# Optimization experiments

Hardware: AMD Instinct MI355X
Metric: run time of the kernel (lower is better)

The kernel has to match this reference:

```python
import jax, jax.numpy as jnp
import numpy as np

K = 100  # number of negative samples
EPS = 1e-6


def setup_inputs() -> dict:
    key = jax.random.key(0)
    k1, k2, k3 = jax.random.split(key, 3)
    B, V = 1024, 100000
    noise_logits = jax.random.normal(k1, (B, V), dtype=jnp.float32)
    actual_logits = jax.random.normal(k2, (B, K + 1), dtype=jnp.float32)
    target_id = jax.random.randint(k3, (B,), 0, V, dtype=jnp.int64)
    return {"noise_logits": noise_logits, "actual_logits": actual_logits, "target_id": target_id}


def reference(noise_logits, actual_logits, target_id):
    B, V = noise_logits.shape
    # Mask the target item out (torch: one_hot scatter then softmax*one_hot, renormalized
    # implicitly by multinomial). Equivalent: set target logit to -inf.
    neg_inf = jnp.finfo(noise_logits.dtype).min
    masked = noise_logits.at[jnp.arange(B), target_id].set(neg_inf)
    # Without-replacement multinomial from softmax(masked) via Gumbel top-k.
    g = jax.random.gumbel(jax.random.key(42), (B, V), dtype=noise_logits.dtype)
    _, neg_items = jax.lax.top_k(masked + g, K)  # [B, K]
    pos_neg_items = jnp.concatenate([target_id[:, None].astype(neg_items.dtype), neg_items], axis=1)  # [B, K+1]
    # Scoring
    noise_prob = jnp.take_along_axis(noise_logits, pos_neg_items, axis=1)  # [B, K+1]
    noise_prob = jax.nn.softmax(noise_prob, axis=-1)
    actual_prob = jax.nn.softmax(actual_logits, axis=-1)
    deno = K * noise_prob + actual_prob + EPS
    tmp1 = actual_prob / deno
    tmp2 = noise_prob / deno
    likeli = jnp.concatenate([tmp1[:, :1], tmp2[:, 1:]], axis=1)
    likeli = jnp.where(likeli == 1.0, 1.0 + EPS, likeli)
    return -jnp.mean(jnp.log(likeli))
```

## Files before the change

kernel.cpp:

```cpp
#include <hip/hip_runtime.h>
#include <stdint.h>

#define NROWS   1024
#define NV      100000
#define NSEL    101
#define NBINS   2048
#define POOLSZ  2048
#define CHUNK   1024
#define NCHUNK  ((NV + CHUNK - 1) / CHUNK)

__device__ __forceinline__ uint32_t rotl32(uint32_t x, uint32_t r) {
  return (x << r) | (x >> (32u - r));
}

__device__ __forceinline__ uint32_t jax_random_bits(uint32_t n) {
  const uint32_t K1 = 42u;
  const uint32_t K2 = 0x1BD11BF0u;
  uint32_t x0 = 0u;
  uint32_t x1 = n + K1;
#define TF_R(r) { x0 += x1; x1 = rotl32(x1, (r)); x1 ^= x0; }
  TF_R(13u) TF_R(15u) TF_R(26u) TF_R(6u)
  x0 += K1; x1 += K2 + 1u;
  TF_R(17u) TF_R(29u) TF_R(16u) TF_R(24u)
  x0 += K2; x1 += 0u + 2u;
  TF_R(13u) TF_R(15u) TF_R(26u) TF_R(6u)
  x0 += 0u; x1 += K1 + 3u;
  TF_R(17u) TF_R(29u) TF_R(16u) TF_R(24u)
  x0 += K1; x1 += K2 + 4u;
  TF_R(13u) TF_R(15u) TF_R(26u) TF_R(6u)
  x0 += K2; x1 += 0u + 5u;
#undef TF_R
  return x0 ^ x1;
}

__device__ __forceinline__ float jax_gumbel(uint32_t n) {
  uint32_t bits = jax_random_bits(n);
  float f = __uint_as_float((bits >> 9) | 0x3f800000u) - 1.0f;
  f = fmaxf(f, 1.1754943508222875e-38f);
  return -__logf(-__logf(f));
}

__device__ __forceinline__ float blk_reduce(float x, int tid, float* wred, bool is_max) {
  #pragma unroll
  for (int off = 32; off >= 1; off >>= 1) {
    float o = __shfl_down(x, off);
    x = is_max ? fmaxf(x, o) : (x + o);
  }
  if ((tid & 63) == 0) wred[tid >> 6] = x;
  __syncthreads();
  float r;
  if (is_max) r = fmaxf(fmaxf(wred[0], wred[1]), fmaxf(wred[2], wred[3]));
  else        r = wred[0] + wred[1] + wred[2] + wred[3];
  __syncthreads();
  return r;
}

__device__ __forceinline__ uint32_t sortable_bin(float v) {
  uint32_t fb = __float_as_uint(v);
  uint32_t key = fb ^ (uint32_t)(((int32_t)fb >> 31) | (int32_t)0x80000000);
  return key >> 21;
}

__global__ void __launch_bounds__(256)
nce_row_kernel(const float* __restrict__ noise, const float* __restrict__ actual,
               const int* __restrict__ target, float* __restrict__ acc) {
  const int row = blockIdx.x;
  const int tid = threadIdx.x;

  __shared__ float    pv[POOLSZ];
  __shared__ uint32_t pi[POOLSZ];
  __shared__ uint32_t hist[NBINS];
  __shared__ uint32_t s_cnt;
  __shared__ uint32_t s_thr;
  __shared__ float    s_wred[4];

  for (int i = tid; i < NBINS; i += 256) hist[i] = 0u;
  if (tid == 0) { s_cnt = 0u; s_thr = 0u; }
  __syncthreads();

  const float* rowp = noise + (size_t)row * NV;
  const uint32_t tgt = (uint32_t)target[row];
  const uint32_t nbase = (uint32_t)row * (uint32_t)NV;

  for (int c = 0; c < NCHUNK; ++c) {
    const uint32_t thr = s_thr;
    const int v = c * CHUNK + tid * 4;
    if (v < NV) {
      float4 a = *reinterpret_cast<const float4*>(rowp + v);
      float av[4] = {a.x, a.y, a.z, a.w};
      #pragma unroll
      for (int j = 0; j < 4; ++j) {
        const uint32_t col = (uint32_t)(v + j);
        const float logit = (col == tgt) ? -3.4028234663852886e+38f : av[j];
        const float val = logit + jax_gumbel(nbase + col);
        const uint32_t bin = sortable_bin(val);
        if (bin >= thr) {
          uint32_t pos = atomicAdd(&s_cnt, 1u);
          if (pos < POOLSZ) { pv[pos] = val; pi[pos] = col; }
          atomicAdd(&hist[bin], 1u);
        }
      }
    }
    __syncthreads();

    if (tid < 64) {
      const int bpl = NBINS / 64;
      uint32_t sum = 0;
      const uint32_t base = (uint32_t)tid * bpl;
      #pragma unroll
      for (int j = 0; j < bpl; ++j) sum += hist[base + j];
      uint32_t suf = sum;
      #pragma unroll
      for (int off = 1; off < 64; off <<= 1) {
        uint32_t o = __shfl_down(suf, off);
        if (tid + off < 64) suf += o;
      }
      const uint32_t sufnext = suf - sum;
      if (suf >= 100u && sufnext < 100u) {
        uint32_t cum = sufnext;
        uint32_t b = base + bpl - 1;
        for (;; --b) { cum += hist[b]; if (cum >= 100u) break; }
        if (b > s_thr) s_thr = b;
      }
    }
    __syncthreads();

    if (s_cnt > (uint32_t)(POOLSZ - CHUNK)) {
      const uint32_t n = min(s_cnt, (uint32_t)POOLSZ);
      const uint32_t thr2 = s_thr;
      float    lv[8]; uint32_t li[8]; int nkeep = 0;
      for (uint32_t p = tid; p < n; p += 256) {
        float val = pv[p];
        if (sortable_bin(val) >= thr2) { lv[nkeep] = val; li[nkeep] = pi[p]; ++nkeep; }
      }
      __syncthreads();
      if (tid == 0) s_cnt = 0u;
      __syncthreads();
      for (int k = 0; k < nkeep; ++k) {
        uint32_t pos = atomicAdd(&s_cnt, 1u);
        if (pos < POOLSZ) { pv[pos] = lv[k]; pi[pos] = li[k]; }
      }
      __syncthreads();
    }
  }
  __syncthreads();

  const uint32_t n = min(s_cnt, (uint32_t)POOLSZ);
  uint32_t sortn = 128;
  while (sortn < n) sortn <<= 1;
  for (uint32_t i = n + tid; i < sortn; i += 256) { pv[i] = -INFINITY; pi[i] = 0xFFFFFFFFu; }
  __syncthreads();

  for (uint32_t ksz = 2; ksz <= sortn; ksz <<= 1) {
    for (uint32_t jsz = ksz >> 1; jsz >= 1; jsz >>= 1) {
      for (uint32_t i = tid; i < sortn; i += 256) {
        const uint32_t ixj = i ^ jsz;
        if (ixj > i) {
          const bool desc = ((i & ksz) == 0);
          float va = pv[i], vb = pv[ixj];
          uint32_t ia = pi[i], ib = pi[ixj];
          const bool a_less = (va < vb) || (va == vb && ia > ib);
          if (desc ? a_less : !a_less) {
            pv[i] = vb; pv[ixj] = va; pi[i] = ib; pi[ixj] = ia;
          }
        }
      }
      __syncthreads();
    }
  }

  float nl = -INFINITY, al = -INFINITY;
  if (tid < NSEL) {
    const uint32_t idx = (tid == 0) ? tgt : pi[tid - 1];
    nl = rowp[idx];
    al = actual[(size_t)row * NSEL + tid];
  }
  const float mn = blk_reduce(nl, tid, s_wred, true);
  const float ma = blk_reduce(al, tid, s_wred, true);
  const float en = (tid < NSEL) ? __expf(nl - mn) : 0.0f;
  const float ea = (tid < NSEL) ? __expf(al - ma) : 0.0f;
  const float sn = blk_reduce(en, tid, s_wred, false);
  const float sa = blk_reduce(ea, tid, s_wred, false);

  float contrib = 0.0f;
  if (tid < NSEL) {
    const float npj = en / sn;
    const float apj = ea / sa;
    const float deno = 100.0f * npj + apj + 1e-6f;
    float t = (tid == 0) ? (apj / deno) : (npj / deno);
    if (t == 1.0f) t = 1.0f + 1e-6f;
    contrib = logf(t);
  }
  const float tot = blk_reduce(contrib, tid, s_wred, false);
  if (tid == 0) atomicAdd(acc, tot);
}

__global__ void zero_acc_kernel(float* acc) {
  if (threadIdx.x == 0 && blockIdx.x == 0) acc[0] = 0.0f;
}

__global__ void finalize_kernel(const float* __restrict__ acc, float* __restrict__ out) {
  if (threadIdx.x == 0 && blockIdx.x == 0)
    out[0] = -acc[0] / (1024.0f * 101.0f);
}

extern "C" void kernel_launch(void* const* d_in, const int* in_sizes, int n_in,
                              void* d_out, int out_size, void* d_ws, size_t ws_size,
                              hipStream_t stream) {
  const float* noise  = (const float*)d_in[0];
  const float* actual = (const float*)d_in[1];
  const int*   target = (const int*)d_in[2];
  float* out = (float*)d_out;
  float* acc = (float*)d_ws;

  zero_acc_kernel<<<1, 64, 0, stream>>>(acc);
  nce_row_kernel<<<NROWS, 256, 0, stream>>>(noise, actual, target, acc);
  finalize_kernel<<<1, 64, 0, stream>>>(acc, out);
}
```

Measured before the change: 910.3 us.

## Double block size, prefetch next chunk, aggregate pool atomics, fuse finalize

```diff
diff --git a/kernel.cpp b/kernel.cpp
--- a/kernel.cpp
+++ b/kernel.cpp
@@ -5,8 +5,9 @@
 #define NV      100000
 #define NSEL    101
 #define NBINS   2048
-#define POOLSZ  2048
-#define CHUNK   1024
+#define POOLSZ  3072
+#define NTHR    512
+#define CHUNK   2048
 #define NCHUNK  ((NV + CHUNK - 1) / CHUNK)
 
 __device__ __forceinline__ uint32_t rotl32(uint32_t x, uint32_t r) {
@@ -48,9 +49,10 @@
   }
   if ((tid & 63) == 0) wred[tid >> 6] = x;
   __syncthreads();
-  float r;
-  if (is_max) r = fmaxf(fmaxf(wred[0], wred[1]), fmaxf(wred[2], wred[3]));
-  else        r = wred[0] + wred[1] + wred[2] + wred[3];
+  float r = wred[0];
+  #pragma unroll
+  for (int w = 1; w < NTHR / 64; ++w)
+    r = is_max ? fmaxf(r, wred[w]) : (r + wred[w]);
   __syncthreads();
   return r;
 }
@@ -61,20 +63,22 @@
   return key >> 21;
 }
 
-__global__ void __launch_bounds__(256)
+__global__ void __launch_bounds__(NTHR, 8)
 nce_row_kernel(const float* __restrict__ noise, const float* __restrict__ actual,
-               const int* __restrict__ target, float* __restrict__ acc) {
+               const int* __restrict__ target, float* __restrict__ acc,
+               uint32_t* __restrict__ ticket, float* __restrict__ out) {
   const int row = blockIdx.x;
   const int tid = threadIdx.x;
+  const int lane = tid & 63;
 
   __shared__ float    pv[POOLSZ];
   __shared__ uint32_t pi[POOLSZ];
   __shared__ uint32_t hist[NBINS];
   __shared__ uint32_t s_cnt;
   __shared__ uint32_t s_thr;
-  __shared__ float    s_wred[4];
-
-  for (int i = tid; i < NBINS; i += 256) hist[i] = 0u;
+  __shared__ float    s_wred[NTHR / 64];
+
+  for (int i = tid; i < NBINS; i += NTHR) hist[i] = 0u;
   if (tid == 0) { s_cnt = 0u; s_thr = 0u; }
   __syncthreads();
 
@@ -82,20 +86,39 @@
   const uint32_t tgt = (uint32_t)target[row];
   const uint32_t nbase = (uint32_t)row * (uint32_t)NV;
 
+  float4 a;
+  {
+    const int v0 = tid * 4;
+    if (v0 < NV) a = *reinterpret_cast<const float4*>(rowp + v0);
+  }
+
   for (int c = 0; c < NCHUNK; ++c) {
+    float4 a_next;
+    {
+      const int vn = (c + 1) * CHUNK + tid * 4;
+      if (c + 1 < NCHUNK && vn < NV)
+        a_next = *reinterpret_cast<const float4*>(rowp + vn);
+    }
+
     const uint32_t thr = s_thr;
     const int v = c * CHUNK + tid * 4;
-    if (v < NV) {
-      float4 a = *reinterpret_cast<const float4*>(rowp + v);
-      float av[4] = {a.x, a.y, a.z, a.w};
-      #pragma unroll
-      for (int j = 0; j < 4; ++j) {
-        const uint32_t col = (uint32_t)(v + j);
-        const float logit = (col == tgt) ? -3.4028234663852886e+38f : av[j];
-        const float val = logit + jax_gumbel(nbase + col);
-        const uint32_t bin = sortable_bin(val);
-        if (bin >= thr) {
-          uint32_t pos = atomicAdd(&s_cnt, 1u);
+    const float av[4] = {a.x, a.y, a.z, a.w};
+    #pragma unroll
+    for (int j = 0; j < 4; ++j) {
+      const uint32_t col = (uint32_t)(v + j);
+      const bool valid = (v + j) < NV;
+      const float logit = (col == tgt) ? -3.4028234663852886e+38f : av[j];
+      const float val = logit + jax_gumbel(nbase + col);
+      const uint32_t bin = sortable_bin(val);
+      const bool pred = valid && (bin >= thr);
+      const unsigned long long mask = __ballot(pred);
+      if (mask) {
+        const int leader = __ffsll((long long)mask) - 1;
+        uint32_t base = 0;
+        if (lane == leader) base = atomicAdd(&s_cnt, (uint32_t)__popcll(mask));
+        base = __shfl(base, leader);
+        if (pred) {
+          const uint32_t pos = base + (uint32_t)__popcll(mask & ((1ull << lane) - 1ull));
           if (pos < POOLSZ) { pv[pos] = val; pi[pos] = col; }
           atomicAdd(&hist[bin], 1u);
         }
@@ -128,8 +151,8 @@
     if (s_cnt > (uint32_t)(POOLSZ - CHUNK)) {
       const uint32_t n = min(s_cnt, (uint32_t)POOLSZ);
       const uint32_t thr2 = s_thr;
-      float    lv[8]; uint32_t li[8]; int nkeep = 0;
-      for (uint32_t p = tid; p < n; p += 256) {
+      float lv[POOLSZ / NTHR]; uint32_t li[POOLSZ / NTHR]; int nkeep = 0;
+      for (uint32_t p = tid; p < n; p += NTHR) {
         float val = pv[p];
         if (sortable_bin(val) >= thr2) { lv[nkeep] = val; li[nkeep] = pi[p]; ++nkeep; }
       }
@@ -142,18 +165,19 @@
       }
       __syncthreads();
     }
-  }
-  __syncthreads();
-
-  const uint32_t n = min(s_cnt, (uint32_t)POOLSZ);
+    a = a_next;
+  }
+  __syncthreads();
+
+  const uint32_t n = min(s_cnt, (uint32_t)2048);
   uint32_t sortn = 128;
   while (sortn < n) sortn <<= 1;
-  for (uint32_t i = n + tid; i < sortn; i += 256) { pv[i] = -INFINITY; pi[i] = 0xFFFFFFFFu; }
+  for (uint32_t i = n + tid; i < sortn; i += NTHR) { pv[i] = -INFINITY; pi[i] = 0xFFFFFFFFu; }
   __syncthreads();
 
   for (uint32_t ksz = 2; ksz <= sortn; ksz <<= 1) {
     for (uint32_t jsz = ksz >> 1; jsz >= 1; jsz >>= 1) {
-      for (uint32_t i = tid; i < sortn; i += 256) {
+      for (uint32_t i = tid; i < sortn; i += NTHR) {
         const uint32_t ixj = i ^ jsz;
         if (ixj > i) {
           const bool desc = ((i & ksz) == 0);
@@ -192,16 +216,16 @@
     contrib = logf(t);
   }
   const float tot = blk_reduce(contrib, tid, s_wred, false);
-  if (tid == 0) atomicAdd(acc, tot);
-}
-
-__global__ void zero_acc_kernel(float* acc) {
-  if (threadIdx.x == 0 && blockIdx.x == 0) acc[0] = 0.0f;
-}
-
-__global__ void finalize_kernel(const float* __restrict__ acc, float* __restrict__ out) {
-  if (threadIdx.x == 0 && blockIdx.x == 0)
-    out[0] = -acc[0] / (1024.0f * 101.0f);
+
+  if (tid == 0) {
+    atomicAdd(acc, tot);
+    __threadfence();
+    const uint32_t t = atomicAdd(ticket, 1u);
+    if (t == (uint32_t)(NROWS - 1)) {
+      const float total = atomicAdd(acc, 0.0f) + 0.0f;
+      out[0] = -total / (1024.0f * 101.0f);
+    }
+  }
 }
 
 extern "C" void kernel_launch(void* const* d_in, const int* in_sizes, int n_in,
@@ -211,9 +235,9 @@
   const float* actual = (const float*)d_in[1];
   const int*   target = (const int*)d_in[2];
   float* out = (float*)d_out;
-  float* acc = (float*)d_ws;
-
-  zero_acc_kernel<<<1, 64, 0, stream>>>(acc);
-  nce_row_kernel<<<NROWS, 256, 0, stream>>>(noise, actual, target, acc);
-  finalize_kernel<<<1, 64, 0, stream>>>(acc, out);
-}
+  float*    acc    = (float*)d_ws;
+  uint32_t* ticket = (uint32_t*)d_ws + 1;
+
+  hipMemsetAsync(d_ws, 0, 8, stream);
+  nce_row_kernel<<<NROWS, NTHR, 0, stream>>>(noise, actual, target, acc, ticket, out);
+}
```

Result: faster. 807.6 us (-11.3%).
